# Kernel tuning notes

Measured on AMD Instinct MI355X. Metric: run time of the kernel, lower is better.

## Reference

```python
import jax, jax.numpy as jnp
import numpy as np
from jax import lax

B, C, H, W = 16, 128, 64, 64
S = 16  # d_state


def setup_inputs() -> dict:
    key = jax.random.key(0)
    ks = jax.random.split(key, 12)
    d = {
        'x': jax.random.normal(ks[0], (B, C, H, W), jnp.float32),
        'conv_w': jax.random.normal(ks[1], (C, C, 3, 3), jnp.float32) * (1.0 / np.sqrt(C * 9)),
        'conv_b': jax.random.normal(ks[2], (C,), jnp.float32) * 0.01,
        'dt_w': jax.random.normal(ks[3], (C, C), jnp.float32) * (1.0 / np.sqrt(C)),
        'dt_b': jax.random.normal(ks[4], (C,), jnp.float32) * 0.01,
        'A': jax.random.normal(ks[5], (C, S), jnp.float32),
        'D': jax.random.normal(ks[6], (C,), jnp.float32),
        'g1_w': jax.random.normal(ks[7], (C, C), jnp.float32) * (1.0 / np.sqrt(C)),
        'g1_b': jax.random.normal(ks[8], (C,), jnp.float32) * 0.01,
        'g2_w': jax.random.normal(ks[9], (C, C), jnp.float32) * (1.0 / np.sqrt(C)),
        'g2_b': jax.random.normal(ks[10], (C,), jnp.float32) * 0.01,
    }
    return d


def _forward(x, conv_w, conv_b, dt_w, dt_b, A, D, g1_w, g1_b, g2_w, g2_b):
    identity = x
    # 3x3 conv, padding=1 (SAME)
    x = lax.conv_general_dilated(x, conv_w, (1, 1), 'SAME',
                                 dimension_numbers=('NCHW', 'OIHW', 'NCHW'))
    x = x + conv_b[None, :, None, None]
    # spectral gate: global avg pool -> 1x1 conv -> relu -> 1x1 conv -> sigmoid
    pooled = jnp.mean(x, axis=(2, 3))                       # [B, C]
    g = jax.nn.relu(jnp.einsum('bc,oc->bo', pooled, g1_w) + g1_b)
    g = jax.nn.sigmoid(jnp.einsum('bc,oc->bo', g, g2_w) + g2_b)
    x = x * g[:, :, None, None]
    # ssm scan over H*W tokens
    x_seq = x.transpose(0, 2, 3, 1).reshape(x.shape[0], H * W, C)  # [B, L, C]
    dt = jax.nn.sigmoid(jnp.einsum('blc,oc->blo', x_seq, dt_w) + dt_b)
    An = -jnp.exp(A)   # [C, S]
    Dp = jnp.exp(D)    # [C]

    def step(h, inp):
        xt, dtt = inp  # each [B, C]
        h = h * jnp.exp(An[None] * dtt[:, :, None]) + xt[:, :, None]  # [B, C, S]
        y = jnp.sum(h * An[None], axis=-1) + Dp * xt                   # [B, C]
        return h, y

    h0 = jnp.zeros((x.shape[0], C, S), x.dtype)
    xs = (x_seq.transpose(1, 0, 2), dt.transpose(1, 0, 2))  # [L, B, C]
    _, ys = lax.scan(step, h0, xs)                           # ys: [L, B, C]
    y = ys.transpose(1, 0, 2).reshape(x.shape[0], H, W, C).transpose(0, 3, 1, 2)
    return y + identity


def reference(x, conv_w, conv_b, dt_w, dt_b, A, D, g1_w, g1_b, g2_w, g2_b):
    return _forward(x, conv_w, conv_b, dt_w, dt_b, A, D, g1_w, g1_b, g2_w, g2_b)
```

## Files before the change

kernel.cpp:

```cpp
#include <hip/hip_runtime.h>
#include <hip/hip_bf16.h>
#include <stdint.h>

#define BB 16
#define CC 128
#define HH 64
#define WW 64
#define LL 4096
#define SS 16
#define NCH 64
#define CT 64

typedef __attribute__((ext_vector_type(4))) float f32x4;
typedef __attribute__((ext_vector_type(8))) short short8;
typedef __attribute__((ext_vector_type(4))) unsigned int u32x4;

#define AS1 __attribute__((address_space(1)))
#define AS3 __attribute__((address_space(3)))

__device__ __forceinline__ float bf2f(unsigned short u) {
    union { unsigned int i; float f; } v;
    v.i = ((unsigned int)u) << 16;
    return v.f;
}
__device__ __forceinline__ unsigned short f2bf(float f) {
    union { float f; unsigned int i; } v;
    v.f = f;
    unsigned int x = v.i;
    return (unsigned short)((x + 0x7fffu + ((x >> 16) & 1u)) >> 16);
}
__device__ __forceinline__ float fexp2(float x) { return __builtin_amdgcn_exp2f(x); }

__global__ __launch_bounds__(256) void k0(const float* __restrict__ x, unsigned short* __restrict__ xT,
                                          const float* __restrict__ conv_w, const float* __restrict__ dt_w,
                                          const float* __restrict__ A, const float* __restrict__ Dv,
                                          const float* __restrict__ g1w, const float* __restrict__ g2w,
                                          short* __restrict__ wf, short* __restrict__ wdtf,
                                          float* __restrict__ An, float* __restrict__ An2, float* __restrict__ Dp,
                                          float* __restrict__ pooled, float* __restrict__ g1wT, float* __restrict__ g2wT) {
    __shared__ float lt[64][65];
    int bid = blockIdx.x;
    int tid = threadIdx.x;
    if (bid < 2048) {
        int b = bid >> 7, rem = bid & 127;
        int tt = rem >> 1, ct = rem & 1;
        int t0 = tt * 64, c0 = ct * 64;
        int colr = tid & 63, rowb = tid >> 6;
#pragma unroll
        for (int r = 0; r < 16; ++r) {
            int row = rowb + r * 4;
            lt[row][colr] = x[(size_t)(b * CC + c0 + row) * LL + t0 + colr];
        }
        __syncthreads();
#pragma unroll
        for (int r = 0; r < 16; ++r) {
            int trow = rowb + r * 4;
            xT[((size_t)b * LL + t0 + trow) * CC + c0 + colr] = f2bf(lt[colr][trow]);
        }
        return;
    }
    int idx = (bid - 2048) * 256 + tid;
    if (idx < 18432) {
        int lane = idx & 63, fr = idx >> 6;
        int nfg = fr & 7, ks = (fr >> 3) & 3, tp = fr >> 5;
        int dy = tp / 3, dx = tp % 3;
        int cout = nfg * 16 + (lane & 15);
        int cin0 = ks * 32 + (lane >> 4) * 8;
        short8 v;
#pragma unroll
        for (int j = 0; j < 8; ++j)
            v[j] = (short)f2bf(conv_w[((cout * CC + cin0 + j) * 3 + dy) * 3 + dx]);
        *(short8*)(wf + (size_t)idx * 8) = v;
    } else if (idx < 20480) {
        int i2 = idx - 18432;
        int lane = i2 & 63, fr = i2 >> 6;
        int nfg = fr & 7, ks = fr >> 3;
        int o = nfg * 16 + (lane & 15);
        int c0 = ks * 32 + (lane >> 4) * 8;
        short8 v;
#pragma unroll
        for (int j = 0; j < 8; ++j) v[j] = (short)f2bf(dt_w[o * CC + c0 + j]);
        *(short8*)(wdtf + (size_t)i2 * 8) = v;
    } else if (idx < 22528) {
        int i3 = idx - 20480;
        float a = -expf(A[i3]);
        An[i3] = a;
        An2[i3] = a * 1.4426950408889634f;
    } else if (idx < 22656) {
        int c = idx - 22528;
        Dp[c] = expf(Dv[c]);
    } else if (idx < 24704) {
        pooled[idx - 22656] = 0.f;
    } else if (idx < 41088) {
        int i = idx - 24704;
        int c = i >> 7, o = i & 127;
        g1wT[i] = g1w[o * 128 + c];
    } else if (idx < 57472) {
        int i = idx - 41088;
        int c = i >> 7, o = i & 127;
        g2wT[i] = g2w[o * 128 + c];
    }
}

__global__ __launch_bounds__(256) void k1(const unsigned short* __restrict__ xT,
                                          const short* __restrict__ wf,
                                          const float* __restrict__ conv_b,
                                          unsigned short* __restrict__ convT,
                                          float* __restrict__ pooled) {
    __shared__ __align__(16) unsigned short slab[3 * 66 * 128];
    int bid = blockIdx.x;
    int b = bid >> 6, h = bid & 63;
    int tid = threadIdx.x;
    int wave = tid >> 6, lane = tid & 63;

    if (tid < 96) {
        int dy = tid >> 5, r = (tid >> 4) & 1, j = tid & 15;
        u32x4 z = {0, 0, 0, 0};
        *(u32x4*)((char*)slab + dy * 16896 + (r ? 16640 : 0) + j * 16) = z;
    }
#pragma unroll
    for (int dy = 0; dy < 3; ++dy) {
        int hs = h + dy - 1;
        char* slabdy = (char*)slab + dy * 16896;
        if (hs >= 0 && hs < HH) {
            const char* src = (const char*)xT + (size_t)(b * LL + hs * 64) * 256;
#pragma unroll
            for (int i = 0; i < 4; ++i) {
                unsigned int Xbase = 256u + (unsigned)i * 4096u + (unsigned)wave * 1024u;
                unsigned int X = Xbase + (unsigned)lane * 16u;
                unsigned int tok = X >> 8;
                unsigned int srcoff = ((X & ~255u) - 256u) | ((X & 255u) ^ ((tok & 7u) << 4));
                __builtin_amdgcn_global_load_lds((const AS1 unsigned int*)(src + srcoff),
                                                 (AS3 unsigned int*)(slabdy + Xbase), 16, 0, 0);
            }
        } else {
            u32x4 z = {0, 0, 0, 0};
#pragma unroll
            for (int i = 0; i < 4; ++i)
                *(u32x4*)(slabdy + 256 + tid * 64 + i * 16) = z;
        }
    }
    __syncthreads();

    int lm = lane & 15, lg = lane >> 4;
    f32x4 acc[4][2];
#pragma unroll
    for (int m = 0; m < 4; ++m)
#pragma unroll
        for (int n = 0; n < 2; ++n) acc[m][n] = (f32x4){0.f, 0.f, 0.f, 0.f};

#pragma unroll
    for (int tp = 0; tp < 9; ++tp) {
        int dy = tp / 3, dx = tp % 3;
        const char* slabdy = (const char*)slab + dy * 16896;
#pragma unroll
        for (int ks = 0; ks < 4; ++ks) {
            short8 bf0 = *(const short8*)(wf + ((size_t)(((tp * 4 + ks) * 8) + wave * 2 + 0) * 64 + lane) * 8);
            short8 bf1 = *(const short8*)(wf + ((size_t)(((tp * 4 + ks) * 8) + wave * 2 + 1) * 64 + lane) * 8);
#pragma unroll
            for (int mf = 0; mf < 4; ++mf) {
                int tok = mf * 16 + lm + dx;
                unsigned int off = (unsigned)((tok * 256 + ks * 64 + lg * 16) ^ ((tok & 7) << 4));
                short8 af = *(const short8*)(slabdy + off);
                acc[mf][0] = __builtin_amdgcn_mfma_f32_16x16x32_bf16(af, bf0, acc[mf][0], 0, 0, 0);
                acc[mf][1] = __builtin_amdgcn_mfma_f32_16x16x32_bf16(af, bf1, acc[mf][1], 0, 0, 0);
            }
        }
    }

    int n0w = wave * 32;
    size_t tokbase = (size_t)(b * LL + h * 64);
    float psum[2] = {0.f, 0.f};
#pragma unroll
    for (int nf = 0; nf < 2; ++nf) {
        int n = n0w + nf * 16 + lm;
        float bias = conv_b[n];
#pragma unroll
        for (int mf = 0; mf < 4; ++mf)
#pragma unroll
            for (int r = 0; r < 4; ++r) {
                int w = mf * 16 + lg * 4 + r;
                float v = acc[mf][nf][r] + bias;
                convT[(tokbase + w) * CC + n] = f2bf(v);
                psum[nf] += v;
            }
    }
#pragma unroll
    for (int nf = 0; nf < 2; ++nf) {
        float s = psum[nf];
        s += __shfl_xor(s, 16);
        s += __shfl_xor(s, 32);
        if (lane < 16) atomicAdd(&pooled[b * CC + n0w + nf * 16 + lane], s);
    }
}

__global__ __launch_bounds__(256) void k3(const unsigned short* __restrict__ convT,
                                          const short* __restrict__ wdtf,
                                          const float* __restrict__ pooled,
                                          const float* __restrict__ g1wT, const float* __restrict__ g1b,
                                          const float* __restrict__ g2wT, const float* __restrict__ g2b,
                                          float* __restrict__ gate,
                                          const float* __restrict__ dt_b,
                                          const float* __restrict__ An2,
                                          unsigned short* __restrict__ dtT,
                                          float* __restrict__ hend, float* __restrict__ decay) {
    __shared__ __align__(16) unsigned short albuf[128 * 128];
    __shared__ __align__(16) unsigned short dtl[128 * 136];
    __shared__ float gl[128];
    float* meanr = (float*)dtl;
    float* garr  = ((float*)dtl) + 128;
    int bid = blockIdx.x;
    int b = bid >> 5, tile = bid & 31, t0 = tile * 128;
    int tid = threadIdx.x;
    int wave = tid >> 6, lane = tid & 63;

    if (tid < 128) meanr[tid] = pooled[b * CC + tid] * (1.f / 4096.f);
    __syncthreads();
    if (tid < 128) {
        float acc = g1b[tid];
        for (int c = 0; c < 128; ++c) acc += meanr[c] * g1wT[c * 128 + tid];
        garr[tid] = fmaxf(acc, 0.f);
    }
    __syncthreads();
    if (tid < 128) {
        float acc2 = g2b[tid];
        for (int c = 0; c < 128; ++c) acc2 += garr[c] * g2wT[c * 128 + tid];
        float gv = __builtin_amdgcn_rcpf(1.f + fexp2(-1.4426950408889634f * acc2));
        gl[tid] = gv;
        if (tile == 0) gate[b * CC + tid] = gv;
    }
    __syncthreads();

    const char* srcb = (const char*)convT + (size_t)(b * LL + t0) * 256;
#pragma unroll
    for (int i = 0; i < 8; ++i) {
        unsigned int byteoff = (unsigned)((i * 256 + tid) * 16);
        unsigned int tok = byteoff >> 8;
        unsigned int inner = byteoff & 255u;
        int c8 = (int)(inner >> 1);
        short8 v = *(const short8*)(srcb + (size_t)tok * 256 + inner);
#pragma unroll
        for (int j = 0; j < 8; ++j) {
            float f = bf2f((unsigned short)v[j]) * gl[c8 + j];
            v[j] = (short)f2bf(f);
        }
        *(short8*)((char*)albuf + (byteoff ^ ((tok & 7u) << 4))) = v;
    }
    __syncthreads();

    int lm = lane & 15, lg = lane >> 4;
    f32x4 acc[8][2];
#pragma unroll
    for (int m = 0; m < 8; ++m)
#pragma unroll
        for (int n = 0; n < 2; ++n) acc[m][n] = (f32x4){0.f, 0.f, 0.f, 0.f};
#pragma unroll
    for (int ks = 0; ks < 4; ++ks) {
        short8 bf0 = *(const short8*)(wdtf + ((size_t)((ks * 8) + wave * 2 + 0) * 64 + lane) * 8);
        short8 bf1 = *(const short8*)(wdtf + ((size_t)((ks * 8) + wave * 2 + 1) * 64 + lane) * 8);
#pragma unroll
        for (int mf = 0; mf < 8; ++mf) {
            int tok = mf * 16 + lm;
            unsigned int off = (unsigned)((tok * 256 + ks * 64 + lg * 16) ^ ((tok & 7) << 4));
            short8 af = *(const short8*)((const char*)albuf + off);
            acc[mf][0] = __builtin_amdgcn_mfma_f32_16x16x32_bf16(af, bf0, acc[mf][0], 0, 0, 0);
            acc[mf][1] = __builtin_amdgcn_mfma_f32_16x16x32_bf16(af, bf1, acc[mf][1], 0, 0, 0);
        }
    }
    __syncthreads();
#pragma unroll
    for (int nf = 0; nf < 2; ++nf) {
        int o = wave * 32 + nf * 16 + lm;
        float zb = dt_b[o];
#pragma unroll
        for (int mf = 0; mf < 8; ++mf)
#pragma unroll
            for (int r = 0; r < 4; ++r) {
                int tok = mf * 16 + lg * 4 + r;
                float z = acc[mf][nf][r] + zb;
                float d = __builtin_amdgcn_rcpf(1.f + fexp2(-1.4426950408889634f * z));
                unsigned short ub = f2bf(d);
                dtT[(size_t)(b * LL + t0 + tok) * CC + o] = ub;
                dtl[tok * 136 + o] = ub;
            }
    }
    __syncthreads();

    int half = tid >> 7, c = tid & 127;
    int ch = tile * 2 + half;
    float a2[SS], h[SS];
#pragma unroll
    for (int s = 0; s < SS; ++s) {
        a2[s] = An2[c * SS + s];
        h[s] = 0.f;
    }
    float sdt = 0.f;
#pragma unroll 4
    for (int t = 0; t < CT; ++t) {
        int tokb = half * 64 + t;
        unsigned int xoff = ((unsigned)(tokb * 256 + c * 2)) ^ (((unsigned)tokb & 7u) << 4);
        float x = bf2f(*(const unsigned short*)((const char*)albuf + xoff));
        float d = bf2f(dtl[tokb * 136 + c]);
        sdt += d;
#pragma unroll
        for (int s = 0; s < SS; ++s) h[s] = h[s] * fexp2(a2[s] * d) + x;
    }
    size_t base = ((size_t)(b * NCH + ch) * CC + c) * SS;
#pragma unroll
    for (int q = 0; q < 4; ++q) {
        f32x4 hv, dv;
#pragma unroll
        for (int j = 0; j < 4; ++j) {
            hv[j] = h[q * 4 + j];
            dv[j] = fexp2(a2[q * 4 + j] * sdt);
        }
        *(f32x4*)(hend + base + q * 4) = hv;
        *(f32x4*)(decay + base + q * 4) = dv;
    }
}

__global__ __launch_bounds__(256) void k5(const float* __restrict__ hend, const float* __restrict__ decay,
                                          float* __restrict__ H0) {
    int idx = blockIdx.x * 256 + threadIdx.x;
    int b = idx >> 11, rem = idx & 2047;
    float Hv = 0.f;
    for (int k = 0; k < NCH; ++k) {
        size_t base = (size_t)(b * NCH + k) * 2048 + rem;
        H0[base] = Hv;
        Hv = hend[base] + Hv * decay[base];
    }
}

__global__ __launch_bounds__(128) void k6(const unsigned short* __restrict__ convT,
                                          const unsigned short* __restrict__ dtT,
                                          const float* __restrict__ gate,
                                          const float* __restrict__ Antab,
                                          const float* __restrict__ An2tab,
                                          const float* __restrict__ Dp,
                                          const float* __restrict__ H0,
                                          const float* __restrict__ xin,
                                          float* __restrict__ out) {
    __shared__ __align__(16) unsigned short xl[64 * 128];
    __shared__ __align__(16) unsigned short dl[64 * 128];
    __shared__ unsigned short ylds[128][66];
    int bid = blockIdx.x;
    int b = bid >> 6, ch = bid & 63;
    int tid = threadIdx.x;
    int wave = tid >> 6, lane = tid & 63;
    int t0 = ch * CT;

    const char* xsrc = (const char*)convT + (size_t)(b * LL + t0) * 256;
    const char* dsrc = (const char*)dtT + (size_t)(b * LL + t0) * 256;
#pragma unroll
    for (int i = 0; i < 8; ++i) {
        unsigned int off = (unsigned)(i * 2048 + wave * 1024);
        __builtin_amdgcn_global_load_lds((const AS1 unsigned int*)(xsrc + off + lane * 16u),
                                         (AS3 unsigned int*)((char*)xl + off), 16, 0, 0);
        __builtin_amdgcn_global_load_lds((const AS1 unsigned int*)(dsrc + off + lane * 16u),
                                         (AS3 unsigned int*)((char*)dl + off), 16, 0, 0);
    }

    int c = tid;
    float a2[SS], an[SS], h[SS];
#pragma unroll
    for (int s = 0; s < SS; ++s) {
        a2[s] = An2tab[c * SS + s];
        an[s] = Antab[c * SS + s];
    }
    size_t hbase = ((size_t)(b * NCH + ch) * CC + c) * SS;
#pragma unroll
    for (int q = 0; q < 4; ++q) {
        f32x4 hv = *(const f32x4*)(H0 + hbase + q * 4);
#pragma unroll
        for (int j = 0; j < 4; ++j) h[q * 4 + j] = hv[j];
    }
    float g = gate[b * CC + c];
    float dpc = Dp[c];
    __syncthreads();

#pragma unroll 4
    for (int t = 0; t < CT; ++t) {
        float x = bf2f(xl[t * 128 + c]) * g;
        float d = bf2f(dl[t * 128 + c]);
        float y = dpc * x;
#pragma unroll
        for (int s = 0; s < SS; ++s) {
            h[s] = h[s] * fexp2(a2[s] * d) + x;
            y += h[s] * an[s];
        }
        ylds[c][t] = f2bf(y);
    }
    __syncthreads();

    int tt = lane;
    size_t outbase = (size_t)b * CC * LL + t0 + tt;
#pragma unroll 4
    for (int rr = 0; rr < 64; ++rr) {
        int row = rr * 2 + wave;
        size_t gi = outbase + (size_t)row * LL;
        out[gi] = bf2f(ylds[row][tt]) + xin[gi];
    }
}

extern "C" void kernel_launch(void* const* d_in, const int* in_sizes, int n_in,
                              void* d_out, int out_size, void* d_ws, size_t ws_size,
                              hipStream_t stream) {
    const float* x      = (const float*)d_in[0];
    const float* conv_w = (const float*)d_in[1];
    const float* conv_b = (const float*)d_in[2];
    const float* dt_w   = (const float*)d_in[3];
    const float* dt_b   = (const float*)d_in[4];
    const float* A      = (const float*)d_in[5];
    const float* D      = (const float*)d_in[6];
    const float* g1w    = (const float*)d_in[7];
    const float* g1b    = (const float*)d_in[8];
    const float* g2w    = (const float*)d_in[9];
    const float* g2b    = (const float*)d_in[10];

    char* ws = (char*)d_ws;
    unsigned short* xT    = (unsigned short*)(ws + 0);
    float* hend           = (float*)(ws + 0);
    float* decay          = (float*)(ws + 8388608);
    unsigned short* convT = (unsigned short*)(ws + 16777216);
    unsigned short* dtT   = (unsigned short*)(ws + 33554432);
    float* H0             = (float*)(ws + 50331648);
    float* g1wT           = (float*)(ws + 50331648);
    float* g2wT           = (float*)(ws + 50397184);
    short* wf             = (short*)(ws + 58720256);
    short* wdtf           = (short*)(ws + 59015168);
    float* pooled         = (float*)(ws + 59047936);
    float* gate           = (float*)(ws + 59056128);
    float* Antab          = (float*)(ws + 59064320);
    float* An2tab         = (float*)(ws + 59072512);
    float* Dp             = (float*)(ws + 59080704);
    float* outp           = (float*)d_out;

    hipLaunchKernelGGL(k0, dim3(2273), dim3(256), 0, stream, x, xT, conv_w, dt_w, A, D, g1w, g2w,
                       wf, wdtf, Antab, An2tab, Dp, pooled, g1wT, g2wT);
    hipLaunchKernelGGL(k1, dim3(1024), dim3(256), 0, stream, xT, wf, conv_b, convT, pooled);
    hipLaunchKernelGGL(k3, dim3(512), dim3(256), 0, stream, convT, wdtf, pooled, g1wT, g1b, g2wT, g2b,
                       gate, dt_b, An2tab, dtT, hend, decay);
    hipLaunchKernelGGL(k5, dim3(128), dim3(256), 0, stream, hend, decay, H0);
    hipLaunchKernelGGL(k6, dim3(1024), dim3(128), 0, stream, convT, dtT, gate, Antab, An2tab, Dp, H0, x, outp);
}
```

Before: 129.7 us.

## Read scan inputs directly from global memory and split output accumulation

The scan kernel no longer stages the x and dt chunks into LDS with global_load_lds. Each thread now reads its channel's bf16 values straight from global memory inside the time loop, which cuts LDS usage and adds an occupancy hint of 4 blocks. The per-step output reduction over the 16 states is split into four partial accumulators to shorten the dependency chain. The A tables are loaded with vector loads. The risk is that per-step 2-byte global loads add latency on the serial time loop that the LDS prefetch previously hid.

```diff
diff --git a/kernel.cpp b/kernel.cpp
--- a/kernel.cpp
+++ b/kernel.cpp
@@ -331,41 +331,30 @@
     }
 }
 
-__global__ __launch_bounds__(128) void k6(const unsigned short* __restrict__ convT,
-                                          const unsigned short* __restrict__ dtT,
-                                          const float* __restrict__ gate,
-                                          const float* __restrict__ Antab,
-                                          const float* __restrict__ An2tab,
-                                          const float* __restrict__ Dp,
-                                          const float* __restrict__ H0,
-                                          const float* __restrict__ xin,
-                                          float* __restrict__ out) {
-    __shared__ __align__(16) unsigned short xl[64 * 128];
-    __shared__ __align__(16) unsigned short dl[64 * 128];
+__global__ __launch_bounds__(128, 4) void k6(const unsigned short* __restrict__ convT,
+                                             const unsigned short* __restrict__ dtT,
+                                             const float* __restrict__ gate,
+                                             const float* __restrict__ Antab,
+                                             const float* __restrict__ An2tab,
+                                             const float* __restrict__ Dp,
+                                             const float* __restrict__ H0,
+                                             const float* __restrict__ xin,
+                                             float* __restrict__ out) {
     __shared__ unsigned short ylds[128][66];
     int bid = blockIdx.x;
     int b = bid >> 6, ch = bid & 63;
     int tid = threadIdx.x;
     int wave = tid >> 6, lane = tid & 63;
     int t0 = ch * CT;
-
-    const char* xsrc = (const char*)convT + (size_t)(b * LL + t0) * 256;
-    const char* dsrc = (const char*)dtT + (size_t)(b * LL + t0) * 256;
-#pragma unroll
-    for (int i = 0; i < 8; ++i) {
-        unsigned int off = (unsigned)(i * 2048 + wave * 1024);
-        __builtin_amdgcn_global_load_lds((const AS1 unsigned int*)(xsrc + off + lane * 16u),
-                                         (AS3 unsigned int*)((char*)xl + off), 16, 0, 0);
-        __builtin_amdgcn_global_load_lds((const AS1 unsigned int*)(dsrc + off + lane * 16u),
-                                         (AS3 unsigned int*)((char*)dl + off), 16, 0, 0);
-    }
-
     int c = tid;
+
     float a2[SS], an[SS], h[SS];
 #pragma unroll
-    for (int s = 0; s < SS; ++s) {
-        a2[s] = An2tab[c * SS + s];
-        an[s] = Antab[c * SS + s];
+    for (int q = 0; q < 4; ++q) {
+        f32x4 av = *(const f32x4*)(An2tab + c * SS + q * 4);
+        f32x4 nv = *(const f32x4*)(Antab + c * SS + q * 4);
+#pragma unroll
+        for (int j = 0; j < 4; ++j) { a2[q * 4 + j] = av[j]; an[q * 4 + j] = nv[j]; }
     }
     size_t hbase = ((size_t)(b * NCH + ch) * CC + c) * SS;
 #pragma unroll
@@ -376,18 +365,22 @@
     }
     float g = gate[b * CC + c];
     float dpc = Dp[c];
-    __syncthreads();
+    const unsigned short* xp = convT + (size_t)(b * LL + t0) * CC + c;
+    const unsigned short* dp = dtT + (size_t)(b * LL + t0) * CC + c;
 
 #pragma unroll 4
     for (int t = 0; t < CT; ++t) {
-        float x = bf2f(xl[t * 128 + c]) * g;
-        float d = bf2f(dl[t * 128 + c]);
-        float y = dpc * x;
+        float x = bf2f(xp[t * CC]) * g;
+        float d = bf2f(dp[t * CC]);
+        float ys[4];
+#pragma unroll
+        for (int j = 0; j < 4; ++j) ys[j] = 0.f;
 #pragma unroll
         for (int s = 0; s < SS; ++s) {
             h[s] = h[s] * fexp2(a2[s] * d) + x;
-            y += h[s] * an[s];
-        }
+            ys[s & 3] += h[s] * an[s];
+        }
+        float y = dpc * x + ((ys[0] + ys[1]) + (ys[2] + ys[3]));
         ylds[c][t] = f2bf(y);
     }
     __syncthreads();
```

Result: faster. 120.7 us (-6.9%).
